# Kernel tuning notes

Measured on AMD Instinct MI355X. Metric: run time of the kernel, lower is better.

## Reference

```python
import jax, jax.numpy as jnp
import numpy as np

B, T, V, E, H = 64, 32, 32000, 512, 1024  # batch, caption len, vocab, embed, hidden


def setup_inputs() -> dict:
    key = jax.random.key(0)
    ks = jax.random.split(key, 10)
    sV = 1.0 / np.sqrt(V)   # nn.Linear init scale
    sH = 1.0 / np.sqrt(H)   # nn.LSTM init scale
    return {
        "features": jax.random.normal(ks[0], (B, E), jnp.float32),
        "captions": jax.random.randint(ks[1], (B, T), 0, V, dtype=jnp.int32),
        # embed = nn.Linear(vocab_size, embed_size): W [E, V], b [E]
        "W_embed": jax.random.uniform(ks[2], (E, V), jnp.float32, -sV, sV),
        "b_embed": jax.random.uniform(ks[3], (E,), jnp.float32, -sV, sV),
        # single-layer LSTM params, PyTorch gate order (i, f, g, o)
        "w_ih": jax.random.uniform(ks[4], (4 * H, E), jnp.float32, -sH, sH),
        "w_hh": jax.random.uniform(ks[5], (4 * H, H), jnp.float32, -sH, sH),
        "b_ih": jax.random.uniform(ks[6], (4 * H,), jnp.float32, -sH, sH),
        "b_hh": jax.random.uniform(ks[7], (4 * H,), jnp.float32, -sH, sH),
        # the torch module draws these with torch.randn at every call; made explicit here
        "h0": jax.random.normal(ks[8], (B, H), jnp.float32),
        "c0": jax.random.normal(ks[9], (B, H), jnp.float32),
    }


def _lstm(inputs, h0, c0, w_ih, w_hh, b_ih, b_hh):
    # inputs: [B, S, E] -> outputs [B, S, H]
    def step(carry, x_t):
        h, c = carry
        gates = x_t @ w_ih.T + h @ w_hh.T + (b_ih + b_hh)  # [B, 4H]
        i, f, g, o = jnp.split(gates, 4, axis=-1)
        c = jax.nn.sigmoid(f) * c + jax.nn.sigmoid(i) * jnp.tanh(g)
        h = jax.nn.sigmoid(o) * jnp.tanh(c)
        return (h, c), h

    _, hs = jax.lax.scan(step, (h0, c0), jnp.transpose(inputs, (1, 0, 2)))
    return jnp.transpose(hs, (1, 0, 2))


def reference(features, captions, W_embed, b_embed, w_ih, w_hh, b_ih, b_hh, h0, c0):
    # Faithful to the original: expand captions to dense one-hot [B, T, V]
    # and push through the Linear layer (the exact wasteful op pattern under study).
    onehot = jax.nn.one_hot(captions, V, dtype=jnp.float32)       # [B, T, V]
    emb = jnp.einsum("btv,ev->bte", onehot, W_embed) + b_embed     # [B, T, E]
    inputs = jnp.concatenate([features[:, None, :], emb], axis=1)  # [B, T+1, E]
    return _lstm(inputs, h0, c0, w_ih, w_hh, b_ih, b_hh)           # [B, T+1, H]
```

## Files before the change

### kernel.cpp

```cpp
#include <hip/hip_runtime.h>
#include <hip/hip_bf16.h>

#define B_   64
#define T_   32
#define S_   33
#define V_   32000
#define E_   512
#define H_   1024
#define HB_  (B_ * H_)
#define NG_  4096

typedef __attribute__((ext_vector_type(8))) short  bf16x8;
typedef __attribute__((ext_vector_type(4))) float  f32x4;

__device__ inline void split2(float x, unsigned short& hi, unsigned short& lo) {
    __hip_bfloat16 h = __float2bfloat16(x);
    float r = x - __bfloat162float(h);
    __hip_bfloat16 l = __float2bfloat16(r);
    hi = *reinterpret_cast<unsigned short*>(&h);
    lo = *reinterpret_cast<unsigned short*>(&l);
}

__device__ inline void load_f32x8_hilo(const float* __restrict__ p,
                                       bf16x8& hi, bf16x8& lo) {
    const float4* q = reinterpret_cast<const float4*>(p);
    float4 v0 = q[0], v1 = q[1];
    float f[8] = {v0.x, v0.y, v0.z, v0.w, v1.x, v1.y, v1.z, v1.w};
#pragma unroll
    for (int j = 0; j < 8; ++j) {
        unsigned short h, l; split2(f[j], h, l);
        hi[j] = (short)h; lo[j] = (short)l;
    }
}

__device__ inline void load_hpk8(const unsigned int* __restrict__ p,
                                 bf16x8& hi, bf16x8& lo) {
    uint4 v0 = *reinterpret_cast<const uint4*>(p);
    uint4 v1 = *reinterpret_cast<const uint4*>(p + 4);
    unsigned int w[8] = {v0.x, v0.y, v0.z, v0.w, v1.x, v1.y, v1.z, v1.w};
#pragma unroll
    for (int j = 0; j < 8; ++j) {
        hi[j] = (short)(w[j] & 0xffffu);
        lo[j] = (short)(w[j] >> 16);
    }
}

__global__ __launch_bounds__(512) void build_x(
    const float* __restrict__ feat,
    const int*   __restrict__ caps,
    const float* __restrict__ Wemb,
    const float* __restrict__ bemb,
    unsigned short* __restrict__ Xhi,
    unsigned short* __restrict__ Xlo)
{
    int row = blockIdx.x;
    int t = row >> 6, b = row & 63;
    int e = threadIdx.x;
    float x;
    if (t == 0) {
        x = feat[b * E_ + e];
    } else {
        int cap = caps[b * T_ + (t - 1)];
        x = Wemb[(size_t)e * V_ + cap] + bemb[e];
    }
    unsigned short hi, lo; split2(x, hi, lo);
    Xhi[(size_t)row * E_ + e] = hi;
    Xlo[(size_t)row * E_ + e] = lo;
}

__global__ __launch_bounds__(256) void init_state(
    const float* __restrict__ h0,
    const float* __restrict__ c0,
    unsigned int* __restrict__ hseq0,
    float* __restrict__ c,
    unsigned int* __restrict__ flags,
    unsigned int* __restrict__ gen)
{
    int idx = blockIdx.x * 256 + threadIdx.x;
    if (idx < 512 * 32)  flags[idx] = 0u;
    if (idx < 2 * 64 * 32) gen[idx] = 0u;
    unsigned short hi, lo; split2(h0[idx], hi, lo);
    hseq0[idx] = (unsigned int)hi | ((unsigned int)lo << 16);
    c[idx]   = c0[idx];
}

__global__ __launch_bounds__(256) void split_w(
    const float* __restrict__ src,
    unsigned short* __restrict__ hi,
    unsigned short* __restrict__ lo,
    int n4)
{
    int idx = blockIdx.x * 256 + threadIdx.x;
    int stride = gridDim.x * 256;
    for (; idx < n4; idx += stride) {
        float4 v = reinterpret_cast<const float4*>(src)[idx];
        float f[4] = {v.x, v.y, v.z, v.w};
        unsigned short h[4], l[4];
#pragma unroll
        for (int j = 0; j < 4; ++j) split2(f[j], h[j], l[j]);
        ushort4 hv; hv.x = h[0]; hv.y = h[1]; hv.z = h[2]; hv.w = h[3];
        ushort4 lv; lv.x = l[0]; lv.y = l[1]; lv.z = l[2]; lv.w = l[3];
        *reinterpret_cast<ushort4*>(hi + (size_t)idx * 4) = hv;
        *reinterpret_cast<ushort4*>(lo + (size_t)idx * 4) = lv;
    }
}

__global__ __launch_bounds__(256) void bias_sum(
    const float* __restrict__ a, const float* __restrict__ b,
    float* __restrict__ s)
{
    int i = blockIdx.x * 256 + threadIdx.x;
    s[i] = a[i] + b[i];
}

template<bool PRESPLIT>
__global__ __launch_bounds__(256) void gx_gemm(
    const unsigned short* __restrict__ Xhi,
    const unsigned short* __restrict__ Xlo,
    const unsigned short* __restrict__ Wihhi,
    const unsigned short* __restrict__ Wihlo,
    const float* __restrict__ w_ih,
    const float* __restrict__ bsum,
    float* __restrict__ Gxi)
{
    int bx   = blockIdx.x;
    int jg   = bx & 255;
    int m0   = (bx >> 8) * 32;
    int wave = threadIdx.x >> 6;
    int lane = threadIdx.x & 63;
    int lm   = lane & 15;
    int kq   = (lane >> 4) * 8;
    int tid  = threadIdx.x;
    int nrow = (lm >> 2) * H_ + jg * 4 + (lm & 3);
    int k0   = wave * 128;

    const unsigned short* Bhi = nullptr;
    const unsigned short* Blo = nullptr;
    const float* Bf = nullptr;
    if (PRESPLIT) { Bhi = Wihhi + (size_t)nrow * E_; Blo = Wihlo + (size_t)nrow * E_; }
    else          { Bf  = w_ih + (size_t)nrow * E_; }

    f32x4 acc0 = f32x4{0.f, 0.f, 0.f, 0.f};
    f32x4 acc1 = f32x4{0.f, 0.f, 0.f, 0.f};

#pragma unroll
    for (int kk = 0; kk < 128; kk += 32) {
        int k = k0 + kk + kq;
        bf16x8 bhi, blo;
        if constexpr (PRESPLIT) {
            bhi = *reinterpret_cast<const bf16x8*>(Bhi + k);
            blo = *reinterpret_cast<const bf16x8*>(Blo + k);
        } else {
            load_f32x8_hilo(Bf + k, bhi, blo);
        }
        bf16x8 a0h = *reinterpret_cast<const bf16x8*>(Xhi + (size_t)(m0 + lm) * E_ + k);
        bf16x8 a0l = *reinterpret_cast<const bf16x8*>(Xlo + (size_t)(m0 + lm) * E_ + k);
        bf16x8 a1h = *reinterpret_cast<const bf16x8*>(Xhi + (size_t)(m0 + 16 + lm) * E_ + k);
        bf16x8 a1l = *reinterpret_cast<const bf16x8*>(Xlo + (size_t)(m0 + 16 + lm) * E_ + k);
        acc0 = __builtin_amdgcn_mfma_f32_16x16x32_bf16(a0h, bhi, acc0, 0, 0, 0);
        acc0 = __builtin_amdgcn_mfma_f32_16x16x32_bf16(a0l, bhi, acc0, 0, 0, 0);
        acc0 = __builtin_amdgcn_mfma_f32_16x16x32_bf16(a0h, blo, acc0, 0, 0, 0);
        acc1 = __builtin_amdgcn_mfma_f32_16x16x32_bf16(a1h, bhi, acc1, 0, 0, 0);
        acc1 = __builtin_amdgcn_mfma_f32_16x16x32_bf16(a1l, bhi, acc1, 0, 0, 0);
        acc1 = __builtin_amdgcn_mfma_f32_16x16x32_bf16(a1h, blo, acc1, 0, 0, 0);
    }

    __shared__ float pbuf[4][2][16][17];
    int rbase = (lane >> 4) * 4;
#pragma unroll
    for (int r = 0; r < 4; ++r) {
        pbuf[wave][0][rbase + r][lm] = acc0[r];
        pbuf[wave][1][rbase + r][lm] = acc1[r];
    }
    __syncthreads();

    for (int idx = tid; idx < 512; idx += 256) {
        int mt = idx >> 8, rc = idx & 255;
        int row = rc >> 4, col = rc & 15;
        float v = pbuf[0][mt][row][col] + pbuf[1][mt][row][col]
                + pbuf[2][mt][row][col] + pbuf[3][mt][row][col];
        int n = (col >> 2) * H_ + jg * 4 + (col & 3);
        Gxi[(size_t)(m0 + mt * 16 + row) * NG_ + jg * 16 + col] = v + bsum[n];
    }
}

template<bool PRESPLIT>
__global__ __launch_bounds__(256, 2) void lstm_persist(
    const float* __restrict__ Gxi,
    const unsigned short* __restrict__ Whhhi,
    const unsigned short* __restrict__ Whhlo,
    const float* __restrict__ w_hh,
    unsigned int* __restrict__ hseq,
    float* __restrict__ c,
    float* __restrict__ out,
    unsigned int* __restrict__ flags,
    unsigned int* __restrict__ gen)
{
    int bx   = blockIdx.x;
    int jg   = bx & 255;
    int mgrp = bx >> 8;
    int wave = threadIdx.x >> 6;
    int lane = threadIdx.x & 63;
    int lm   = lane & 15;
    int kq   = (lane >> 4) * 8;
    int tid  = threadIdx.x;

    int gbase    = bx & 256;
    bool checker = (bx == gbase);
    unsigned int* mygen = gen + ((size_t)mgrp * 64 + ((bx & 255) >> 2)) * 32;

    int nrow = (lm >> 2) * H_ + jg * 4 + (lm & 3);
    int k0   = wave * 256;

    bf16x8 wh[8], wl[8];
    if constexpr (PRESPLIT) {
        const unsigned short* Bhi = Whhhi + (size_t)nrow * H_ + k0 + kq;
        const unsigned short* Blo = Whhlo + (size_t)nrow * H_ + k0 + kq;
#pragma unroll
        for (int i = 0; i < 8; ++i) {
            wh[i] = *reinterpret_cast<const bf16x8*>(Bhi + i * 32);
            wl[i] = *reinterpret_cast<const bf16x8*>(Blo + i * 32);
        }
    } else {
        const float* Bf = w_hh + (size_t)nrow * H_ + k0 + kq;
#pragma unroll
        for (int i = 0; i < 8; ++i) {
            load_f32x8_hilo(Bf + i * 32, wh[i], wl[i]);
        }
    }

    __shared__ float pbuf[4][2][16][17];
    __shared__ float gbuf[2][16][17];
    int rbase = (lane >> 4) * 4;

    for (int t = 0; t < S_; ++t) {
        const unsigned int* hpk_in = hseq + (size_t)t * HB_;
        unsigned int*      hpk_out = hseq + (size_t)(t + 1) * HB_;
        const unsigned int* hrow0 = hpk_in + (size_t)(mgrp * 32 + lm) * H_ + k0 + kq;
        const unsigned int* hrow1 = hpk_in + (size_t)(mgrp * 32 + 16 + lm) * H_ + k0 + kq;

        float gx_i = 0.f, gx_f = 0.f, gx_g = 0.f, gx_o = 0.f;
        if (tid < 128) {
            int mt = tid >> 6, bl = (tid >> 2) & 15, jj = tid & 3;
            int b = mgrp * 32 + mt * 16 + bl;
            const float* gx = Gxi + (size_t)(t * 64 + b) * NG_ + jg * 16;
            gx_i = gx[ 0 + jj];
            gx_f = gx[ 4 + jj];
            gx_g = gx[ 8 + jj];
            gx_o = gx[12 + jj];
        }

        f32x4 acc0 = f32x4{0.f, 0.f, 0.f, 0.f};
        f32x4 acc1 = f32x4{0.f, 0.f, 0.f, 0.f};

#pragma unroll
        for (int i = 0; i < 8; ++i) {
            bf16x8 a0h, a0l, a1h, a1l;
            load_hpk8(hrow0 + i * 32, a0h, a0l);
            load_hpk8(hrow1 + i * 32, a1h, a1l);
            acc0 = __builtin_amdgcn_mfma_f32_16x16x32_bf16(a0h, wh[i], acc0, 0, 0, 0);
            acc0 = __builtin_amdgcn_mfma_f32_16x16x32_bf16(a0l, wh[i], acc0, 0, 0, 0);
            acc0 = __builtin_amdgcn_mfma_f32_16x16x32_bf16(a0h, wl[i], acc0, 0, 0, 0);
            acc1 = __builtin_amdgcn_mfma_f32_16x16x32_bf16(a1h, wh[i], acc1, 0, 0, 0);
            acc1 = __builtin_amdgcn_mfma_f32_16x16x32_bf16(a1l, wh[i], acc1, 0, 0, 0);
            acc1 = __builtin_amdgcn_mfma_f32_16x16x32_bf16(a1h, wl[i], acc1, 0, 0, 0);
        }

#pragma unroll
        for (int r = 0; r < 4; ++r) {
            pbuf[wave][0][rbase + r][lm] = acc0[r];
            pbuf[wave][1][rbase + r][lm] = acc1[r];
        }
        __syncthreads();

        for (int idx = tid; idx < 512; idx += 256) {
            int mt = idx >> 8, rc = idx & 255;
            int row = rc >> 4, col = rc & 15;
            gbuf[mt][row][col] = pbuf[0][mt][row][col] + pbuf[1][mt][row][col]
                               + pbuf[2][mt][row][col] + pbuf[3][mt][row][col];
        }
        __syncthreads();

        if (tid < 128) {
            int mt = tid >> 6, bl = (tid >> 2) & 15, jj = tid & 3;
            int b = mgrp * 32 + mt * 16 + bl;
            int j = jg * 4 + jj;
            float iv = gbuf[mt][bl][ 0 + jj] + gx_i;
            float fv = gbuf[mt][bl][ 4 + jj] + gx_f;
            float gv = gbuf[mt][bl][ 8 + jj] + gx_g;
            float ov = gbuf[mt][bl][12 + jj] + gx_o;
            float si = 1.f / (1.f + expf(-iv));
            float sf = 1.f / (1.f + expf(-fv));
            float so = 1.f / (1.f + expf(-ov));
            float tg = tanhf(gv);
            size_t cidx = (size_t)b * H_ + j;
            float cn = sf * c[cidx] + si * tg;
            c[cidx] = cn;
            float hn = so * tanhf(cn);
            unsigned short hi, lo; split2(hn, hi, lo);
            __hip_atomic_store(&hpk_out[cidx],
                               (unsigned int)hi | ((unsigned int)lo << 16),
                               __ATOMIC_RELAXED, __HIP_MEMORY_SCOPE_AGENT);
            out[((size_t)b * S_ + t) * H_ + j] = hn;
        }

        __syncthreads();
        unsigned int target = (unsigned int)(t + 1);
        if (!checker) {
            if (tid == 0) {
                __hip_atomic_store(&flags[(size_t)bx * 32], target,
                                   __ATOMIC_RELAXED, __HIP_MEMORY_SCOPE_AGENT);
                while (__hip_atomic_load(mygen, __ATOMIC_RELAXED,
                                         __HIP_MEMORY_SCOPE_AGENT) < target) {
                    __builtin_amdgcn_s_sleep(2);
                }
            }
        } else {
            int fi = gbase + 1 + tid;
            bool need = (tid < 255);
            for (;;) {
                int ok = 1;
                if (need) {
                    ok = (__hip_atomic_load(&flags[(size_t)fi * 32],
                                            __ATOMIC_RELAXED,
                                            __HIP_MEMORY_SCOPE_AGENT) >= target);
                }
                if (__syncthreads_and(ok)) break;
                __builtin_amdgcn_s_sleep(2);
            }
            if (tid < 64) {
                __hip_atomic_store(gen + ((size_t)mgrp * 64 + tid) * 32, target,
                                   __ATOMIC_RELAXED, __HIP_MEMORY_SCOPE_AGENT);
            }
        }
        __syncthreads();
    }
}

template<bool PRESPLIT>
__global__ __launch_bounds__(256) void lstm_step(
    const float* __restrict__ Gxi,
    const unsigned short* __restrict__ Whhhi,
    const unsigned short* __restrict__ Whhlo,
    const float* __restrict__ w_hh,
    const unsigned int* __restrict__ hpk_in,
    float* __restrict__ c,
    unsigned int* __restrict__ hpk_out,
    float* __restrict__ out,
    int t)
{
    int bx   = blockIdx.x;
    int jg   = bx & 255;
    int mgrp = bx >> 8;
    int wave = threadIdx.x >> 6;
    int lane = threadIdx.x & 63;
    int lm   = lane & 15;
    int kq   = (lane >> 4) * 8;
    int tid  = threadIdx.x;
    int nrow = (lm >> 2) * H_ + jg * 4 + (lm & 3);
    int k0   = wave * 256;

    const unsigned short* Bhi = nullptr;
    const unsigned short* Blo = nullptr;
    const float* Bf = nullptr;
    if (PRESPLIT) { Bhi = Whhhi + (size_t)nrow * H_; Blo = Whhlo + (size_t)nrow * H_; }
    else          { Bf  = w_hh + (size_t)nrow * H_; }

    const unsigned int* hrow0 = hpk_in + (size_t)(mgrp * 32 + lm) * H_;
    const unsigned int* hrow1 = hpk_in + (size_t)(mgrp * 32 + 16 + lm) * H_;

    f32x4 acc0 = f32x4{0.f, 0.f, 0.f, 0.f};
    f32x4 acc1 = f32x4{0.f, 0.f, 0.f, 0.f};

#pragma unroll
    for (int kk = 0; kk < 256; kk += 32) {
        int k = k0 + kk + kq;
        bf16x8 bhi, blo;
        if constexpr (PRESPLIT) {
            bhi = *reinterpret_cast<const bf16x8*>(Bhi + k);
            blo = *reinterpret_cast<const bf16x8*>(Blo + k);
        } else {
            load_f32x8_hilo(Bf + k, bhi, blo);
        }
        bf16x8 a0h, a0l, a1h, a1l;
        load_hpk8(hrow0 + k, a0h, a0l);
        load_hpk8(hrow1 + k, a1h, a1l);
        acc0 = __builtin_amdgcn_mfma_f32_16x16x32_bf16(a0h, bhi, acc0, 0, 0, 0);
        acc0 = __builtin_amdgcn_mfma_f32_16x16x32_bf16(a0l, bhi, acc0, 0, 0, 0);
        acc0 = __builtin_amdgcn_mfma_f32_16x16x32_bf16(a0h, blo, acc0, 0, 0, 0);
        acc1 = __builtin_amdgcn_mfma_f32_16x16x32_bf16(a1h, bhi, acc1, 0, 0, 0);
        acc1 = __builtin_amdgcn_mfma_f32_16x16x32_bf16(a1l, bhi, acc1, 0, 0, 0);
        acc1 = __builtin_amdgcn_mfma_f32_16x16x32_bf16(a1h, blo, acc1, 0, 0, 0);
    }

    __shared__ float pbuf[4][2][16][17];
    __shared__ float gbuf[2][16][17];
    int rbase = (lane >> 4) * 4;
#pragma unroll
    for (int r = 0; r < 4; ++r) {
        pbuf[wave][0][rbase + r][lm] = acc0[r];
        pbuf[wave][1][rbase + r][lm] = acc1[r];
    }
    __syncthreads();

    for (int idx = tid; idx < 512; idx += 256) {
        int mt = idx >> 8, rc = idx & 255;
        int row = rc >> 4, col = rc & 15;
        gbuf[mt][row][col] = pbuf[0][mt][row][col] + pbuf[1][mt][row][col]
                           + pbuf[2][mt][row][col] + pbuf[3][mt][row][col];
    }
    __syncthreads();

    if (tid < 128) {
        int mt = tid >> 6, bl = (tid >> 2) & 15, jj = tid & 3;
        int b = mgrp * 32 + mt * 16 + bl;
        int j = jg * 4 + jj;
        const float* gx = Gxi + (size_t)(t * 64 + b) * NG_ + jg * 16;
        float iv = gbuf[mt][bl][ 0 + jj] + gx[ 0 + jj];
        float fv = gbuf[mt][bl][ 4 + jj] + gx[ 4 + jj];
        float gv = gbuf[mt][bl][ 8 + jj] + gx[ 8 + jj];
        float ov = gbuf[mt][bl][12 + jj] + gx[12 + jj];
        float si = 1.f / (1.f + expf(-iv));
        float sf = 1.f / (1.f + expf(-fv));
        float so = 1.f / (1.f + expf(-ov));
        float tg = tanhf(gv);
        size_t cidx = (size_t)b * H_ + j;
        float cn = sf * c[cidx] + si * tg;
        c[cidx] = cn;
        float hn = so * tanhf(cn);
        unsigned short hi, lo; split2(hn, hi, lo);
        hpk_out[cidx] = (unsigned int)hi | ((unsigned int)lo << 16);
        out[((size_t)b * S_ + t) * H_ + j] = hn;
    }
}

extern "C" void kernel_launch(void* const* d_in, const int* in_sizes, int n_in,
                              void* d_out, int out_size, void* d_ws, size_t ws_size,
                              hipStream_t stream)
{
    const float* feat = (const float*)d_in[0];
    const int*   caps = (const int*)d_in[1];
    const float* Wemb = (const float*)d_in[2];
    const float* bemb = (const float*)d_in[3];
    const float* w_ih = (const float*)d_in[4];
    const float* w_hh = (const float*)d_in[5];
    const float* b_ih = (const float*)d_in[6];
    const float* b_hh = (const float*)d_in[7];
    const float* h0   = (const float*)d_in[8];
    const float* c0   = (const float*)d_in[9];
    int nbias = 0, nstate = 0;
    for (int i = 0; i < n_in; ++i) {
        switch (in_sizes[i]) {
            case 64 * 512:        feat = (const float*)d_in[i]; break;
            case 64 * 32:         caps = (const int*)d_in[i];   break;
            case 512 * 32000:     Wemb = (const float*)d_in[i]; break;
            case 512:             bemb = (const float*)d_in[i]; break;
            case 4096 * 512:      w_ih = (const float*)d_in[i]; break;
            case 4096 * 1024:     w_hh = (const float*)d_in[i]; break;
            case 4096:
                if (nbias++ == 0) b_ih = (const float*)d_in[i];
                else              b_hh = (const float*)d_in[i];
                break;
            case 64 * 1024:
                if (nstate++ == 0) h0 = (const float*)d_in[i];
                else               c0 = (const float*)d_in[i];
                break;
            default: break;
        }
    }
    float* out = (float*)d_out;

    char* ws = (char*)d_ws;
    unsigned short* Xhi  = (unsigned short*)ws; ws += (size_t)2112 * 512 * 2;
    unsigned short* Xlo  = (unsigned short*)ws; ws += (size_t)2112 * 512 * 2;
    float* Gxi           = (float*)ws;          ws += (size_t)2112 * NG_ * 4;
    unsigned int* hseq   = (unsigned int*)ws;   ws += (size_t)(S_ + 1) * HB_ * 4;
    float* cbuf          = (float*)ws;          ws += (size_t)B_ * H_ * 4;
    float* bsum          = (float*)ws;          ws += (size_t)4096 * 4;
    unsigned int* flags  = (unsigned int*)ws;   ws += (size_t)512 * 32 * 4;
    unsigned int* gen    = (unsigned int*)ws;   ws += (size_t)2 * 64 * 32 * 4;
    unsigned short* Wihhi = (unsigned short*)ws; ws += (size_t)4096 * 512 * 2;
    unsigned short* Wihlo = (unsigned short*)ws; ws += (size_t)4096 * 512 * 2;
    unsigned short* Whhhi = (unsigned short*)ws; ws += (size_t)4096 * 1024 * 2;
    unsigned short* Whhlo = (unsigned short*)ws; ws += (size_t)4096 * 1024 * 2;
    size_t needed = (size_t)(ws - (char*)d_ws);
    bool presplit = ws_size >= needed;

    build_x<<<2112, 512, 0, stream>>>(feat, caps, Wemb, bemb, Xhi, Xlo);
    init_state<<<256, 256, 0, stream>>>(h0, c0, hseq, cbuf, flags, gen);
    bias_sum<<<16, 256, 0, stream>>>(b_ih, b_hh, bsum);
    if (presplit) {
        split_w<<<2048, 256, 0, stream>>>(w_ih, Wihhi, Wihlo, (4096 * 512) / 4);
        split_w<<<2048, 256, 0, stream>>>(w_hh, Whhhi, Whhlo, (4096 * 1024) / 4);
        gx_gemm<true><<<66 * 256, 256, 0, stream>>>(Xhi, Xlo, Wihhi, Wihlo,
                                                    w_ih, bsum, Gxi);
    } else {
        gx_gemm<false><<<66 * 256, 256, 0, stream>>>(Xhi, Xlo, Wihhi, Wihlo,
                                                     w_ih, bsum, Gxi);
    }

    void* args[] = {
        (void*)&Gxi,
        (void*)&Whhhi, (void*)&Whhlo, (void*)&w_hh,
        (void*)&hseq, (void*)&cbuf, (void*)&out,
        (void*)&flags, (void*)&gen
    };
    const void* pk = presplit ? (const void*)lstm_persist<true>
                              : (const void*)lstm_persist<false>;
    hipError_t err = hipLaunchCooperativeKernel(pk, dim3(512), dim3(256),
                                                args, 0, stream);
    if (err != hipSuccess) {
        (void)hipGetLastError();
        for (int t = 0; t < S_; ++t) {
            const unsigned int* hin = hseq + (size_t)t * HB_;
            unsigned int*      hout = hseq + (size_t)(t + 1) * HB_;
            if (presplit) {
                lstm_step<true><<<512, 256, 0, stream>>>(
                    Gxi, Whhhi, Whhlo, w_hh, hin, cbuf, hout, out, t);
            } else {
                lstm_step<false><<<512, 256, 0, stream>>>(
                    Gxi, Whhhi, Whhlo, w_hh, hin, cbuf, hout, out, t);
            }
        }
    }
}
```

Measured before the change: 695.7 us.

## Drop weight pre-split kernels, keep W_ih in registers, prefetch Gx in LSTM loop

Removes the split_w passes that converted w_ih and w_hh into hi/lo bf16 buffers. Each kernel now splits the fp32 weights on load. The input GEMM becomes a 512-block kernel that holds its W_ih slice in registers and loops over 33 row tiles, instead of 16896 blocks that each reload the weights. The persistent LSTM kernel prefetches the next step's Gx values while waiting at the grid barrier. The aim is to save the extra weight-conversion traffic and launches, at the cost of less parallelism in the input GEMM.

```diff
diff --git a/kernel.cpp b/kernel.cpp
--- a/kernel.cpp
+++ b/kernel.cpp
@@ -77,34 +77,13 @@
     unsigned int* __restrict__ gen)
 {
     int idx = blockIdx.x * 256 + threadIdx.x;
-    if (idx < 512 * 32)  flags[idx] = 0u;
-    if (idx < 2 * 64 * 32) gen[idx] = 0u;
+    if (idx < 512 * 32)    flags[idx] = 0u;
+    if (idx < 2 * 64 * 32) gen[idx]   = 0u;
     unsigned short hi, lo; split2(h0[idx], hi, lo);
     hseq0[idx] = (unsigned int)hi | ((unsigned int)lo << 16);
     c[idx]   = c0[idx];
 }
 
-__global__ __launch_bounds__(256) void split_w(
-    const float* __restrict__ src,
-    unsigned short* __restrict__ hi,
-    unsigned short* __restrict__ lo,
-    int n4)
-{
-    int idx = blockIdx.x * 256 + threadIdx.x;
-    int stride = gridDim.x * 256;
-    for (; idx < n4; idx += stride) {
-        float4 v = reinterpret_cast<const float4*>(src)[idx];
-        float f[4] = {v.x, v.y, v.z, v.w};
-        unsigned short h[4], l[4];
-#pragma unroll
-        for (int j = 0; j < 4; ++j) split2(f[j], h[j], l[j]);
-        ushort4 hv; hv.x = h[0]; hv.y = h[1]; hv.z = h[2]; hv.w = h[3];
-        ushort4 lv; lv.x = l[0]; lv.y = l[1]; lv.z = l[2]; lv.w = l[3];
-        *reinterpret_cast<ushort4*>(hi + (size_t)idx * 4) = hv;
-        *reinterpret_cast<ushort4*>(lo + (size_t)idx * 4) = lv;
-    }
-}
-
 __global__ __launch_bounds__(256) void bias_sum(
     const float* __restrict__ a, const float* __restrict__ b,
     float* __restrict__ s)
@@ -113,82 +92,80 @@
     s[i] = a[i] + b[i];
 }
 
-template<bool PRESPLIT>
-__global__ __launch_bounds__(256) void gx_gemm(
+__global__ __launch_bounds__(256, 2) void gx_gemm(
     const unsigned short* __restrict__ Xhi,
     const unsigned short* __restrict__ Xlo,
-    const unsigned short* __restrict__ Wihhi,
-    const unsigned short* __restrict__ Wihlo,
     const float* __restrict__ w_ih,
     const float* __restrict__ bsum,
     float* __restrict__ Gxi)
 {
-    int bx   = blockIdx.x;
-    int jg   = bx & 255;
-    int m0   = (bx >> 8) * 32;
-    int wave = threadIdx.x >> 6;
-    int lane = threadIdx.x & 63;
-    int lm   = lane & 15;
-    int kq   = (lane >> 4) * 8;
-    int tid  = threadIdx.x;
-    int nrow = (lm >> 2) * H_ + jg * 4 + (lm & 3);
-    int k0   = wave * 128;
-
-    const unsigned short* Bhi = nullptr;
-    const unsigned short* Blo = nullptr;
-    const float* Bf = nullptr;
-    if (PRESPLIT) { Bhi = Wihhi + (size_t)nrow * E_; Blo = Wihlo + (size_t)nrow * E_; }
-    else          { Bf  = w_ih + (size_t)nrow * E_; }
-
-    f32x4 acc0 = f32x4{0.f, 0.f, 0.f, 0.f};
-    f32x4 acc1 = f32x4{0.f, 0.f, 0.f, 0.f};
-
-#pragma unroll
-    for (int kk = 0; kk < 128; kk += 32) {
-        int k = k0 + kk + kq;
-        bf16x8 bhi, blo;
-        if constexpr (PRESPLIT) {
-            bhi = *reinterpret_cast<const bf16x8*>(Bhi + k);
-            blo = *reinterpret_cast<const bf16x8*>(Blo + k);
-        } else {
-            load_f32x8_hilo(Bf + k, bhi, blo);
-        }
-        bf16x8 a0h = *reinterpret_cast<const bf16x8*>(Xhi + (size_t)(m0 + lm) * E_ + k);
-        bf16x8 a0l = *reinterpret_cast<const bf16x8*>(Xlo + (size_t)(m0 + lm) * E_ + k);
-        bf16x8 a1h = *reinterpret_cast<const bf16x8*>(Xhi + (size_t)(m0 + 16 + lm) * E_ + k);
-        bf16x8 a1l = *reinterpret_cast<const bf16x8*>(Xlo + (size_t)(m0 + 16 + lm) * E_ + k);
-        acc0 = __builtin_amdgcn_mfma_f32_16x16x32_bf16(a0h, bhi, acc0, 0, 0, 0);
-        acc0 = __builtin_amdgcn_mfma_f32_16x16x32_bf16(a0l, bhi, acc0, 0, 0, 0);
-        acc0 = __builtin_amdgcn_mfma_f32_16x16x32_bf16(a0h, blo, acc0, 0, 0, 0);
-        acc1 = __builtin_amdgcn_mfma_f32_16x16x32_bf16(a1h, bhi, acc1, 0, 0, 0);
-        acc1 = __builtin_amdgcn_mfma_f32_16x16x32_bf16(a1l, bhi, acc1, 0, 0, 0);
-        acc1 = __builtin_amdgcn_mfma_f32_16x16x32_bf16(a1h, blo, acc1, 0, 0, 0);
-    }
+    int bx    = blockIdx.x;
+    int jg    = bx & 255;
+    int mhalf = bx >> 8;
+    int wave  = threadIdx.x >> 6;
+    int lane  = threadIdx.x & 63;
+    int lm    = lane & 15;
+    int kq    = (lane >> 4) * 8;
+    int tid   = threadIdx.x;
+    int nrow  = (lm >> 2) * H_ + jg * 4 + (lm & 3);
+    int k0    = wave * 128;
+
+    bf16x8 wh[4], wl[4];
+    {
+        const float* Bf = w_ih + (size_t)nrow * E_ + k0 + kq;
+#pragma unroll
+        for (int i = 0; i < 4; ++i) load_f32x8_hilo(Bf + i * 32, wh[i], wl[i]);
+    }
+#pragma unroll
+    for (int i = 0; i < 4; ++i)
+        asm volatile("" : "+v"(wh[i]), "+v"(wl[i]));
+
+    int colt = tid & 15;
+    float bias0 = bsum[(colt >> 2) * H_ + jg * 4 + (colt & 3)];
 
     __shared__ float pbuf[4][2][16][17];
     int rbase = (lane >> 4) * 4;
-#pragma unroll
-    for (int r = 0; r < 4; ++r) {
-        pbuf[wave][0][rbase + r][lm] = acc0[r];
-        pbuf[wave][1][rbase + r][lm] = acc1[r];
-    }
-    __syncthreads();
-
-    for (int idx = tid; idx < 512; idx += 256) {
-        int mt = idx >> 8, rc = idx & 255;
-        int row = rc >> 4, col = rc & 15;
-        float v = pbuf[0][mt][row][col] + pbuf[1][mt][row][col]
-                + pbuf[2][mt][row][col] + pbuf[3][mt][row][col];
-        int n = (col >> 2) * H_ + jg * 4 + (col & 3);
-        Gxi[(size_t)(m0 + mt * 16 + row) * NG_ + jg * 16 + col] = v + bsum[n];
-    }
-}
-
-template<bool PRESPLIT>
+
+    for (int mt2 = 0; mt2 < 33; ++mt2) {
+        int m0 = mhalf * 1056 + mt2 * 32;
+
+        f32x4 acc0 = f32x4{0.f, 0.f, 0.f, 0.f};
+        f32x4 acc1 = f32x4{0.f, 0.f, 0.f, 0.f};
+#pragma unroll
+        for (int i = 0; i < 4; ++i) {
+            int k = k0 + i * 32 + kq;
+            bf16x8 a0h = *reinterpret_cast<const bf16x8*>(Xhi + (size_t)(m0 + lm) * E_ + k);
+            bf16x8 a0l = *reinterpret_cast<const bf16x8*>(Xlo + (size_t)(m0 + lm) * E_ + k);
+            bf16x8 a1h = *reinterpret_cast<const bf16x8*>(Xhi + (size_t)(m0 + 16 + lm) * E_ + k);
+            bf16x8 a1l = *reinterpret_cast<const bf16x8*>(Xlo + (size_t)(m0 + 16 + lm) * E_ + k);
+            acc0 = __builtin_amdgcn_mfma_f32_16x16x32_bf16(a0h, wh[i], acc0, 0, 0, 0);
+            acc0 = __builtin_amdgcn_mfma_f32_16x16x32_bf16(a0l, wh[i], acc0, 0, 0, 0);
+            acc0 = __builtin_amdgcn_mfma_f32_16x16x32_bf16(a0h, wl[i], acc0, 0, 0, 0);
+            acc1 = __builtin_amdgcn_mfma_f32_16x16x32_bf16(a1h, wh[i], acc1, 0, 0, 0);
+            acc1 = __builtin_amdgcn_mfma_f32_16x16x32_bf16(a1l, wh[i], acc1, 0, 0, 0);
+            acc1 = __builtin_amdgcn_mfma_f32_16x16x32_bf16(a1h, wl[i], acc1, 0, 0, 0);
+        }
+
+#pragma unroll
+        for (int r = 0; r < 4; ++r) {
+            pbuf[wave][0][rbase + r][lm] = acc0[r];
+            pbuf[wave][1][rbase + r][lm] = acc1[r];
+        }
+        __syncthreads();
+
+        for (int idx = tid; idx < 512; idx += 256) {
+            int mt = idx >> 8;
+            int row = (idx & 255) >> 4, col = idx & 15;
+            float v = pbuf[0][mt][row][col] + pbuf[1][mt][row][col]
+                    + pbuf[2][mt][row][col] + pbuf[3][mt][row][col];
+            Gxi[(size_t)(m0 + mt * 16 + row) * NG_ + jg * 16 + col] = v + bias0;
+        }
+        __syncthreads();
+    }
+}
+
 __global__ __launch_bounds__(256, 2) void lstm_persist(
     const float* __restrict__ Gxi,
-    const unsigned short* __restrict__ Whhhi,
-    const unsigned short* __restrict__ Whhlo,
     const float* __restrict__ w_hh,
     unsigned int* __restrict__ hseq,
     float* __restrict__ c,
@@ -213,42 +190,38 @@
     int k0   = wave * 256;
 
     bf16x8 wh[8], wl[8];
-    if constexpr (PRESPLIT) {
-        const unsigned short* Bhi = Whhhi + (size_t)nrow * H_ + k0 + kq;
-        const unsigned short* Blo = Whhlo + (size_t)nrow * H_ + k0 + kq;
-#pragma unroll
-        for (int i = 0; i < 8; ++i) {
-            wh[i] = *reinterpret_cast<const bf16x8*>(Bhi + i * 32);
-            wl[i] = *reinterpret_cast<const bf16x8*>(Blo + i * 32);
-        }
-    } else {
+    {
         const float* Bf = w_hh + (size_t)nrow * H_ + k0 + kq;
 #pragma unroll
-        for (int i = 0; i < 8; ++i) {
-            load_f32x8_hilo(Bf + i * 32, wh[i], wl[i]);
-        }
-    }
+        for (int i = 0; i < 8; ++i) load_f32x8_hilo(Bf + i * 32, wh[i], wl[i]);
+    }
+#pragma unroll
+    for (int i = 0; i < 8; ++i)
+        asm volatile("" : "+v"(wh[i]), "+v"(wl[i]));
 
     __shared__ float pbuf[4][2][16][17];
     __shared__ float gbuf[2][16][17];
     int rbase = (lane >> 4) * 4;
+
+    float gx_i = 0.f, gx_f = 0.f, gx_g = 0.f, gx_o = 0.f;
+    int pmt = tid >> 6, pbl = (tid >> 2) & 15, pjj = tid & 3;
+    int pb  = mgrp * 32 + pmt * 16 + pbl;
+    auto prefetch_gx = [&](int t) {
+        if (tid < 128) {
+            const float* gx = Gxi + (size_t)(t * 64 + pb) * NG_ + jg * 16;
+            gx_i = gx[ 0 + pjj];
+            gx_f = gx[ 4 + pjj];
+            gx_g = gx[ 8 + pjj];
+            gx_o = gx[12 + pjj];
+        }
+    };
+    prefetch_gx(0);
 
     for (int t = 0; t < S_; ++t) {
         const unsigned int* hpk_in = hseq + (size_t)t * HB_;
         unsigned int*      hpk_out = hseq + (size_t)(t + 1) * HB_;
         const unsigned int* hrow0 = hpk_in + (size_t)(mgrp * 32 + lm) * H_ + k0 + kq;
         const unsigned int* hrow1 = hpk_in + (size_t)(mgrp * 32 + 16 + lm) * H_ + k0 + kq;
-
-        float gx_i = 0.f, gx_f = 0.f, gx_g = 0.f, gx_o = 0.f;
-        if (tid < 128) {
-            int mt = tid >> 6, bl = (tid >> 2) & 15, jj = tid & 3;
-            int b = mgrp * 32 + mt * 16 + bl;
-            const float* gx = Gxi + (size_t)(t * 64 + b) * NG_ + jg * 16;
-            gx_i = gx[ 0 + jj];
-            gx_f = gx[ 4 + jj];
-            gx_g = gx[ 8 + jj];
-            gx_o = gx[12 + jj];
-        }
 
         f32x4 acc0 = f32x4{0.f, 0.f, 0.f, 0.f};
         f32x4 acc1 = f32x4{0.f, 0.f, 0.f, 0.f};
@@ -282,13 +255,12 @@
         __syncthreads();
 
         if (tid < 128) {
-            int mt = tid >> 6, bl = (tid >> 2) & 15, jj = tid & 3;
-            int b = mgrp * 32 + mt * 16 + bl;
-            int j = jg * 4 + jj;
-            float iv = gbuf[mt][bl][ 0 + jj] + gx_i;
-            float fv = gbuf[mt][bl][ 4 + jj] + gx_f;
-            float gv = gbuf[mt][bl][ 8 + jj] + gx_g;
-            float ov = gbuf[mt][bl][12 + jj] + gx_o;
+            int b = pb;
+            int j = jg * 4 + pjj;
+            float iv = gbuf[pmt][pbl][ 0 + pjj] + gx_i;
+            float fv = gbuf[pmt][pbl][ 4 + pjj] + gx_f;
+            float gv = gbuf[pmt][pbl][ 8 + pjj] + gx_g;
+            float ov = gbuf[pmt][pbl][12 + pjj] + gx_o;
             float si = 1.f / (1.f + expf(-iv));
             float sf = 1.f / (1.f + expf(-fv));
             float so = 1.f / (1.f + expf(-ov));
@@ -310,12 +282,16 @@
             if (tid == 0) {
                 __hip_atomic_store(&flags[(size_t)bx * 32], target,
                                    __ATOMIC_RELAXED, __HIP_MEMORY_SCOPE_AGENT);
+            }
+            if (t + 1 < S_) prefetch_gx(t + 1);
+            if (tid == 0) {
                 while (__hip_atomic_load(mygen, __ATOMIC_RELAXED,
                                          __HIP_MEMORY_SCOPE_AGENT) < target) {
                     __builtin_amdgcn_s_sleep(2);
                 }
             }
         } else {
+            if (t + 1 < S_) prefetch_gx(t + 1);
             int fi = gbase + 1 + tid;
             bool need = (tid < 255);
             for (;;) {
@@ -337,11 +313,8 @@
     }
 }
 
-template<bool PRESPLIT>
 __global__ __launch_bounds__(256) void lstm_step(
     const float* __restrict__ Gxi,
-    const unsigned short* __restrict__ Whhhi,
-    const unsigned short* __restrict__ Whhlo,
     const float* __restrict__ w_hh,
     const unsigned int* __restrict__ hpk_in,
     float* __restrict__ c,
@@ -360,12 +333,7 @@
     int nrow = (lm >> 2) * H_ + jg * 4 + (lm & 3);
     int k0   = wave * 256;
 
-    const unsigned short* Bhi = nullptr;
-    const unsigned short* Blo = nullptr;
-    const float* Bf = nullptr;
-    if (PRESPLIT) { Bhi = Whhhi + (size_t)nrow * H_; Blo = Whhlo + (size_t)nrow * H_; }
-    else          { Bf  = w_hh + (size_t)nrow * H_; }
-
+    const float* Bf = w_hh + (size_t)nrow * H_;
     const unsigned int* hrow0 = hpk_in + (size_t)(mgrp * 32 + lm) * H_;
     const unsigned int* hrow1 = hpk_in + (size_t)(mgrp * 32 + 16 + lm) * H_;
 
@@ -376,12 +344,7 @@
     for (int kk = 0; kk < 256; kk += 32) {
         int k = k0 + kk + kq;
         bf16x8 bhi, blo;
-        if constexpr (PRESPLIT) {
-            bhi = *reinterpret_cast<const bf16x8*>(Bhi + k);
-            blo = *reinterpret_cast<const bf16x8*>(Blo + k);
-        } else {
-            load_f32x8_hilo(Bf + k, bhi, blo);
-        }
+        load_f32x8_hilo(Bf + k, bhi, blo);
         bf16x8 a0h, a0l, a1h, a1l;
         load_hpk8(hrow0 + k, a0h, a0l);
         load_hpk8(hrow1 + k, a1h, a1l);
@@ -479,48 +442,27 @@
     float* bsum          = (float*)ws;          ws += (size_t)4096 * 4;
     unsigned int* flags  = (unsigned int*)ws;   ws += (size_t)512 * 32 * 4;
     unsigned int* gen    = (unsigned int*)ws;   ws += (size_t)2 * 64 * 32 * 4;
-    unsigned short* Wihhi = (unsigned short*)ws; ws += (size_t)4096 * 512 * 2;
-    unsigned short* Wihlo = (unsigned short*)ws; ws += (size_t)4096 * 512 * 2;
-    unsigned short* Whhhi = (unsigned short*)ws; ws += (size_t)4096 * 1024 * 2;
-    unsigned short* Whhlo = (unsigned short*)ws; ws += (size_t)4096 * 1024 * 2;
-    size_t needed = (size_t)(ws - (char*)d_ws);
-    bool presplit = ws_size >= needed;
 
     build_x<<<2112, 512, 0, stream>>>(feat, caps, Wemb, bemb, Xhi, Xlo);
     init_state<<<256, 256, 0, stream>>>(h0, c0, hseq, cbuf, flags, gen);
     bias_sum<<<16, 256, 0, stream>>>(b_ih, b_hh, bsum);
-    if (presplit) {
-        split_w<<<2048, 256, 0, stream>>>(w_ih, Wihhi, Wihlo, (4096 * 512) / 4);
-        split_w<<<2048, 256, 0, stream>>>(w_hh, Whhhi, Whhlo, (4096 * 1024) / 4);
-        gx_gemm<true><<<66 * 256, 256, 0, stream>>>(Xhi, Xlo, Wihhi, Wihlo,
-                                                    w_ih, bsum, Gxi);
-    } else {
-        gx_gemm<false><<<66 * 256, 256, 0, stream>>>(Xhi, Xlo, Wihhi, Wihlo,
-                                                     w_ih, bsum, Gxi);
-    }
+    gx_gemm<<<512, 256, 0, stream>>>(Xhi, Xlo, w_ih, bsum, Gxi);
 
     void* args[] = {
-        (void*)&Gxi,
-        (void*)&Whhhi, (void*)&Whhlo, (void*)&w_hh,
+        (void*)&Gxi, (void*)&w_hh,
         (void*)&hseq, (void*)&cbuf, (void*)&out,
         (void*)&flags, (void*)&gen
     };
-    const void* pk = presplit ? (const void*)lstm_persist<true>
-                              : (const void*)lstm_persist<false>;
-    hipError_t err = hipLaunchCooperativeKernel(pk, dim3(512), dim3(256),
+    hipError_t err = hipLaunchCooperativeKernel((const void*)lstm_persist,
+                                                dim3(512), dim3(256),
                                                 args, 0, stream);
     if (err != hipSuccess) {
         (void)hipGetLastError();
         for (int t = 0; t < S_; ++t) {
             const unsigned int* hin = hseq + (size_t)t * HB_;
             unsigned int*      hout = hseq + (size_t)(t + 1) * HB_;
-            if (presplit) {
-                lstm_step<true><<<512, 256, 0, stream>>>(
-                    Gxi, Whhhi, Whhlo, w_hh, hin, cbuf, hout, out, t);
-            } else {
-                lstm_step<false><<<512, 256, 0, stream>>>(
-                    Gxi, Whhhi, Whhlo, w_hh, hin, cbuf, hout, out, t);
-            }
-        }
-    }
-}
+            lstm_step<<<512, 256, 0, stream>>>(
+                Gxi, w_hh, hin, cbuf, hout, out, t);
+        }
+    }
+}
```

New measurement: 648.4 us. 1.07x faster.
